# Kernel tuning notes

Measured on AMD Instinct MI355X. Metric: run time of the kernel, lower is better.

The kernel has to match this reference:

```python
import jax, jax.numpy as jnp
import numpy as np

NUM_HEADS = 16


def setup_inputs() -> dict:
    key = jax.random.key(0)
    ks = jax.random.split(key, 7)
    B, S, H = 2, 2048, 1024
    x = jax.random.normal(ks[0], (B, S, H), dtype=jnp.float32)
    y = jax.random.normal(ks[1], (B, S, H), dtype=jnp.float32)
    bias = jnp.zeros((B, 1, 1, S), dtype=jnp.float32)  # additive attention bias (padding mask)
    w_scale = 0.02
    wq = jax.random.normal(ks[2], (H, H), dtype=jnp.float32) * w_scale
    wk = jax.random.normal(ks[3], (H, H), dtype=jnp.float32) * w_scale
    wv = jax.random.normal(ks[4], (H, H), dtype=jnp.float32) * w_scale
    wo = jax.random.normal(ks[5], (H, H), dtype=jnp.float32) * w_scale
    return {"x": x, "y": y, "bias": bias, "wq": wq, "wk": wk, "wv": wv, "wo": wo}


def reference(x, y, bias, wq, wk, wv, wo):
    B, S, H = x.shape
    nh = NUM_HEADS
    dh = H // nh
    # QKV projections, split heads: [B, S, H] -> [B, nh, S, dh]
    q = jnp.einsum("bsh,hd->bsd", x, wq).reshape(B, S, nh, dh).transpose(0, 2, 1, 3)
    k = jnp.einsum("bsh,hd->bsd", y, wk).reshape(B, S, nh, dh).transpose(0, 2, 1, 3)
    v = jnp.einsum("bsh,hd->bsd", y, wv).reshape(B, S, nh, dh).transpose(0, 2, 1, 3)
    # Scale queries (tensor2tensor convention: q *= size_per_head ** -0.5)
    q = q * (dh ** -0.5)
    logits = jnp.einsum("bhqd,bhkd->bhqk", q, k) + bias  # [B, nh, S, S]
    weights = jax.nn.softmax(logits, axis=-1)
    # (attention_dropout = 0.0 -> identity)
    ctx = jnp.einsum("bhqk,bhkd->bhqd", weights, v)  # [B, nh, S, dh]
    ctx = ctx.transpose(0, 2, 1, 3).reshape(B, S, H)  # combine heads
    return jnp.einsum("bsh,hd->bsd", ctx, wo)
```

## Files before the change

kernel.cpp:

```cpp
#include <hip/hip_runtime.h>

using u16 = unsigned short;
using u32 = unsigned int;

typedef __bf16 bf16x8 __attribute__((ext_vector_type(8)));
typedef __bf16 bf16x4 __attribute__((ext_vector_type(4)));
typedef float f32x4 __attribute__((ext_vector_type(4)));
typedef u16 u16x4 __attribute__((ext_vector_type(4)));

#define GLD_LDS16(gp, lp)                                                                 \
  __builtin_amdgcn_global_load_lds((const __attribute__((address_space(1))) void*)(gp),   \
                                   (__attribute__((address_space(3))) void*)(lp), 16, 0, 0)

__device__ __forceinline__ u16 f2b(float f) {
  union { float f; u32 u; } v; v.f = f;
  return (u16)((v.u + 0x7fffu + ((v.u >> 16) & 1u)) >> 16);
}

__device__ __forceinline__ void pl32swap(u32& a, u32& b) {
  asm("v_permlane32_swap_b32 %0, %1" : "+v"(a), "+v"(b));
}
__device__ __forceinline__ void pl16swap(u32& a, u32& b) {
  asm("v_permlane16_swap_b32 %0, %1" : "+v"(a), "+v"(b));
}
__device__ __forceinline__ u32 cvtpk(float lo, float hi) {
  u32 d; asm("v_cvt_pk_bf16_f32 %0, %1, %2" : "=v"(d) : "v"(lo), "v"(hi));
  return d;
}

__global__ __launch_bounds__(256) void transpose4(
    const float* __restrict__ w0, const float* __restrict__ w1,
    const float* __restrict__ w2, const float* __restrict__ w3,
    u16* __restrict__ o0, u16* __restrict__ o1,
    u16* __restrict__ o2, u16* __restrict__ o3) {
  const float* src; u16* dst;
  switch (blockIdx.z) {
    case 0: src = w0; dst = o0; break;
    case 1: src = w1; dst = o1; break;
    case 2: src = w2; dst = o2; break;
    default: src = w3; dst = o3; break;
  }
  __shared__ float tile[64][65];
  int bx = blockIdx.x * 64, by = blockIdx.y * 64;
  int tx = threadIdx.x & 63, ty = threadIdx.x >> 6;
  for (int r = ty; r < 64; r += 4)
    tile[r][tx] = src[(size_t)(by + r) * 1024 + bx + tx];
  __syncthreads();
  for (int r = ty; r < 64; r += 4)
    dst[(size_t)(bx + r) * 1024 + by + tx] = f2b(tile[tx][r]);
}

__global__ __launch_bounds__(256) void cvt2bf16(
    const float* __restrict__ a, const float* __restrict__ b,
    u16* __restrict__ oa, u16* __restrict__ ob) {
  const float* src = blockIdx.y ? b : a;
  u16* dst = blockIdx.y ? ob : oa;
  size_t i = ((size_t)blockIdx.x * 256 + threadIdx.x) * 8;
  float4 f0 = *(const float4*)(src + i);
  float4 f1 = *(const float4*)(src + i + 4);
  bf16x8 v;
  v[0] = (__bf16)f0.x; v[1] = (__bf16)f0.y; v[2] = (__bf16)f0.z; v[3] = (__bf16)f0.w;
  v[4] = (__bf16)f1.x; v[5] = (__bf16)f1.y; v[6] = (__bf16)f1.z; v[7] = (__bf16)f1.w;
  *(bf16x8*)(dst + i) = v;
}

#define BM 128
#define BN 128
#define BK 64

__global__ __launch_bounds__(256) void gemm_qkv(
    const u16* __restrict__ xb, const u16* __restrict__ yb, const u16* __restrict__ wT,
    u16* __restrict__ Qb, u16* __restrict__ Kb, u16* __restrict__ Vb) {
  __shared__ __align__(16) u16 As[BM * BK];
  __shared__ __align__(16) u16 Bs[BN * BK];
  const int K = 1024;
  int region = blockIdx.y >> 3;
  const u16* A = (region == 0) ? xb : yb;
  const u16* BT = wT + (size_t)region * 1024 * 1024;
  float scale = (region == 0) ? 0.125f : 1.0f;
  int tid = threadIdx.x;
  int wave = tid >> 6, lane = tid & 63;
  int r = lane & 15, kg = lane >> 4;
  int bm = blockIdx.x * BM, bn = (blockIdx.y & 7) * BN;
  int wr = (wave >> 1) * 64, wc = (wave & 1) * 64;
  f32x4 acc[4][4] = {};

  const u16* Ag = A + (size_t)(bm + wave * 32 + (lane >> 3)) * K + (lane & 7) * 8;
  const u16* Bg = BT + (size_t)(bn + wave * 32 + (lane >> 3)) * K + (lane & 7) * 8;
  u16* Asb = As + wave * 32 * BK;
  u16* Bsb = Bs + wave * 32 * BK;

  for (int k0 = 0; k0 < K; k0 += BK) {
#pragma unroll
    for (int c = 0; c < 4; ++c) {
      GLD_LDS16(Ag + (size_t)c * 8 * K + k0, Asb + c * 8 * BK);
      GLD_LDS16(Bg + (size_t)c * 8 * K + k0, Bsb + c * 8 * BK);
    }
    __syncthreads();
#pragma unroll
    for (int kk = 0; kk < 2; ++kk) {
      bf16x8 af[4], bfv[4];
#pragma unroll
      for (int m = 0; m < 4; ++m)
        af[m] = *(const bf16x8*)&As[(wr + m * 16 + r) * BK + kk * 32 + kg * 8];
#pragma unroll
      for (int n = 0; n < 4; ++n)
        bfv[n] = *(const bf16x8*)&Bs[(wc + n * 16 + r) * BK + kk * 32 + kg * 8];
#pragma unroll
      for (int m = 0; m < 4; ++m)
#pragma unroll
        for (int n = 0; n < 4; ++n)
          acc[m][n] = __builtin_amdgcn_mfma_f32_16x16x32_bf16(af[m], bfv[n], acc[m][n], 0, 0, 0);
    }
    __syncthreads();
  }

  if (region == 2) {
#pragma unroll
    for (int m = 0; m < 4; ++m)
#pragma unroll
      for (int n = 0; n < 4; ++n) {
        int row0 = bm + wr + m * 16 + kg * 4;
        int col = bn + wc + n * 16 + r;
        int bb = row0 >> 11, s = row0 & 2047;
        int hh = col >> 6, dd = col & 63;
        u16x4 pk;
#pragma unroll
        for (int i = 0; i < 4; ++i) pk[i] = f2b(acc[m][n][i]);
        *(u16x4*)&Vb[((size_t)(bb * 16 + hh) * 64 + dd) * 2048 + s] = pk;
      }
  } else {
    u16* dst = (region == 0) ? Qb : Kb;
#pragma unroll
    for (int m = 0; m < 4; ++m)
#pragma unroll
      for (int n = 0; n < 4; ++n)
#pragma unroll
        for (int i = 0; i < 4; ++i) {
          int row = bm + wr + m * 16 + kg * 4 + i;
          int col = bn + wc + n * 16 + r;
          dst[(size_t)row * 1024 + col] = f2b(acc[m][n][i] * scale);
        }
  }
}

__global__ __launch_bounds__(256) void gemm_wo(
    const u16* __restrict__ A, const u16* __restrict__ BT, float* __restrict__ Cp,
    float scale) {
  __shared__ __align__(16) u16 As[BM * BK];
  __shared__ __align__(16) u16 Bs[64 * BK];
  const int K = 1024, N = 1024;
  int tid = threadIdx.x;
  int wave = tid >> 6, lane = tid & 63;
  int r = lane & 15, kg = lane >> 4;
  int lhi = lane >> 3, llo = lane & 7;
  int bm = blockIdx.x * BM, bn = blockIdx.y * 64;
  int wr = (wave >> 1) * 64, wc = (wave & 1) * 32;
  f32x4 acc[4][2] = {};

  const u16* Ag = A + (size_t)(bm + wave * 32 + lhi) * K + llo * 8;
  const u16* Bg = BT + (size_t)(bn + wave * 16 + lhi) * K + llo * 8;
  u16* Asb = As + wave * 32 * BK;
  u16* Bsb = Bs + wave * 16 * BK;

  for (int k0 = 0; k0 < K; k0 += BK) {
#pragma unroll
    for (int c = 0; c < 4; ++c)
      GLD_LDS16(Ag + (size_t)c * 8 * K + k0, Asb + c * 8 * BK);
#pragma unroll
    for (int c = 0; c < 2; ++c)
      GLD_LDS16(Bg + (size_t)c * 8 * K + k0, Bsb + c * 8 * BK);
    __syncthreads();
#pragma unroll
    for (int kk = 0; kk < 2; ++kk) {
      bf16x8 af[4], bfv[2];
#pragma unroll
      for (int m = 0; m < 4; ++m)
        af[m] = *(const bf16x8*)&As[(wr + m * 16 + r) * BK + kk * 32 + kg * 8];
#pragma unroll
      for (int n = 0; n < 2; ++n)
        bfv[n] = *(const bf16x8*)&Bs[(wc + n * 16 + r) * BK + kk * 32 + kg * 8];
#pragma unroll
      for (int m = 0; m < 4; ++m)
#pragma unroll
        for (int n = 0; n < 2; ++n)
          acc[m][n] = __builtin_amdgcn_mfma_f32_16x16x32_bf16(af[m], bfv[n], acc[m][n], 0, 0, 0);
    }
    __syncthreads();
  }

#pragma unroll
  for (int m = 0; m < 4; ++m)
#pragma unroll
    for (int n = 0; n < 2; ++n)
#pragma unroll
      for (int i = 0; i < 4; ++i) {
        int row = bm + wr + m * 16 + kg * 4 + i;
        int col = bn + wc + n * 16 + r;
        Cp[(size_t)row * N + col] = acc[m][n][i] * scale;
      }
}

__global__ __launch_bounds__(256) void flash_attn(
    const u16* __restrict__ Q, const u16* __restrict__ Km, const u16* __restrict__ VtG,
    const float* __restrict__ bias, u16* __restrict__ ctx) {
  const int S = 2048, H = 1024;
  __shared__ __align__(16) u16 Ks[2][64 * 64];
  __shared__ __align__(16) u16 Vs[2][64 * 64];
  int tid = threadIdx.x;
  int wave = tid >> 6, lane = tid & 63;
  int r = lane & 15, kg = lane >> 4;
  int h = blockIdx.x, b = blockIdx.y, qt = blockIdx.z;

  bf16x8 qa[2][2];
#pragma unroll
  for (int g = 0; g < 2; ++g) {
    const u16* Qb =
        Q + (size_t)(b * S + qt * 128 + g * 64 + wave * 16 + r) * H + h * 64 + kg * 8;
    qa[g][0] = *(const bf16x8*)(Qb);
    qa[g][1] = *(const bf16x8*)(Qb + 32);
  }

  int lhi = lane >> 3, llo = lane & 7;
  int ksch = llo ^ lhi;
  const u16* KgB = Km + (size_t)b * S * H + h * 64;
  const u16* VgB = VtG + ((size_t)(b * 16 + h) * 64) * 2048;
  const float* biasB = bias + (size_t)b * S;

  float m_i[2] = {-1e30f, -1e30f}, l_i[2] = {0.f, 0.f};
  f32x4 acc[2][4] = {};

  auto issueKV = [&](int kv0, int bi) {
#pragma unroll
    for (int c = 0; c < 2; ++c) {
      GLD_LDS16(KgB + (size_t)(kv0 + wave * 16 + c * 8 + lhi) * H + ksch * 8,
                &Ks[bi][wave * 16 * 64 + c * 8 * 64]);
      GLD_LDS16(VgB + (size_t)(wave * 16 + c * 8 + lhi) * 2048 + kv0 + ksch * 8,
                &Vs[bi][wave * 16 * 64 + c * 8 * 64]);
    }
  };
  auto issueB = [&](int kv0, f32x4* bv) {
#pragma unroll
    for (int n = 0; n < 4; ++n)
      bv[n] = *(const f32x4*)(biasB + kv0 + n * 16 + (kg << 2));
  };

  auto compute = [&](const u16* KsB, const u16* VsB, const f32x4* bv) {
#pragma unroll
    for (int g = 0; g < 2; ++g) {
      f32x4 sv[4] = {};
      __builtin_amdgcn_s_setprio(1);
#pragma unroll
      for (int kk = 0; kk < 2; ++kk)
#pragma unroll
        for (int n = 0; n < 4; ++n) {
          bf16x8 kb = *(const bf16x8*)&KsB[(n * 16 + r) * 64 +
                                           ((((kk << 2) + kg) ^ (r & 7)) << 3)];
          sv[n] = __builtin_amdgcn_mfma_f32_16x16x32_bf16(kb, qa[g][kk], sv[n], 0, 0, 0);
        }
      __builtin_amdgcn_s_setprio(0);

      f32x4 s4[4];
#pragma unroll
      for (int n = 0; n < 4; ++n) s4[n] = sv[n] + bv[n];
      float m0 = fmaxf(fmaxf(s4[0][0], s4[0][1]), fmaxf(s4[0][2], s4[0][3]));
      float m1 = fmaxf(fmaxf(s4[1][0], s4[1][1]), fmaxf(s4[1][2], s4[1][3]));
      float m2 = fmaxf(fmaxf(s4[2][0], s4[2][1]), fmaxf(s4[2][2], s4[2][3]));
      float m3 = fmaxf(fmaxf(s4[3][0], s4[3][1]), fmaxf(s4[3][2], s4[3][3]));
      float mx = fmaxf(fmaxf(m0, m1), fmaxf(m2, m3));
      mx = fmaxf(mx, __shfl_xor(mx, 16));
      mx = fmaxf(mx, __shfl_xor(mx, 32));
      float sc = 1.f;
      if (mx > m_i[g] + 8.f) { sc = __expf(m_i[g] - mx); l_i[g] *= sc; m_i[g] = mx; }
      if (__any(sc != 1.f)) {
#pragma unroll
        for (int i = 0; i < 4; ++i) {
          float sci = __shfl(sc, (lane & 48) | ((kg << 2) + i));
#pragma unroll
          for (int n = 0; n < 4; ++n) acc[g][n][i] *= sci;
        }
      }
      float rs = 0.f;
      float e[4][4];
#pragma unroll
      for (int n = 0; n < 4; ++n)
#pragma unroll
        for (int i = 0; i < 4; ++i) {
          e[n][i] = __expf(s4[n][i] - m_i[g]);
          rs += e[n][i];
        }
      rs += __shfl_xor(rs, 16);
      rs += __shfl_xor(rs, 32);
      l_i[g] += rs;

      u32 w[4][2];
#pragma unroll
      for (int n = 0; n < 4; ++n) {
        w[n][0] = cvtpk(e[n][0], e[n][1]);
        w[n][1] = cvtpk(e[n][2], e[n][3]);
      }

      __builtin_amdgcn_s_setprio(1);
#pragma unroll
      for (int kk = 0; kk < 2; ++kk) {
        u32 a0 = w[2 * kk][0], a1 = w[2 * kk][1];
        u32 b0 = w[2 * kk + 1][0], b1 = w[2 * kk + 1][1];
        pl32swap(a0, b0); pl32swap(a1, b1);
        pl16swap(a0, b0); pl16swap(a1, b1);
        union { u32 u[4]; bf16x8 v; } pa;
        pa.u[0] = a0; pa.u[1] = a1; pa.u[2] = b0; pa.u[3] = b1;
#pragma unroll
        for (int n = 0; n < 4; ++n) {
          bf16x8 vb = *(const bf16x8*)&VsB[(n * 16 + r) * 64 +
                                           ((((kk << 2) + kg) ^ (r & 7)) << 3)];
          acc[g][n] = __builtin_amdgcn_mfma_f32_16x16x32_bf16(pa.v, vb, acc[g][n], 0, 0, 0);
        }
      }
      __builtin_amdgcn_s_setprio(0);
    }
  };

  f32x4 bp[4], bn2[4];

  issueKV(0, 0); issueB(0, bp);
  __syncthreads();

  for (int t2 = 0; t2 < 16; ++t2) {
    int kv1 = (t2 * 2 + 1) * 64;
    int kv2 = ((t2 * 2 + 2) & 31) * 64;
    issueKV(kv1, 1); issueB(kv1, bn2);
    compute(Ks[0], Vs[0], bp);
    __syncthreads();
    issueKV(kv2, 0); issueB(kv2, bp);
    compute(Ks[1], Vs[1], bn2);
    __syncthreads();
  }

#pragma unroll
  for (int g = 0; g < 2; ++g)
#pragma unroll
    for (int i = 0; i < 4; ++i) {
      float li = __shfl(l_i[g], (lane & 48) | ((kg << 2) + i));
      float inv = 1.0f / li;
      size_t row = (size_t)(b * S + qt * 128 + g * 64 + wave * 16 + (kg << 2) + i);
#pragma unroll
      for (int n = 0; n < 4; ++n)
        ctx[row * H + h * 64 + n * 16 + r] = f2b(acc[g][n][i] * inv);
    }
}

extern "C" void kernel_launch(void* const* d_in, const int* in_sizes, int n_in,
                              void* d_out, int out_size, void* d_ws, size_t ws_size,
                              hipStream_t stream) {
  const float* x    = (const float*)d_in[0];
  const float* y    = (const float*)d_in[1];
  const float* bias = (const float*)d_in[2];
  const float* wq   = (const float*)d_in[3];
  const float* wk   = (const float*)d_in[4];
  const float* wv   = (const float*)d_in[5];
  const float* wo   = (const float*)d_in[6];
  float* out = (float*)d_out;

  u16* ws = (u16*)d_ws;
  const size_t WELEM = 1024 * 1024;
  const size_t MELEM = (size_t)4096 * 1024;
  u16* wqT = ws;
  u16* wkT = wqT + WELEM;
  u16* wvT = wkT + WELEM;
  u16* woT = wvT + WELEM;
  u16* Qb  = woT + WELEM;
  u16* Kb  = Qb + MELEM;
  u16* Vb  = Kb + MELEM;
  u16* xb  = Vb + MELEM;
  u16* yb  = xb + MELEM;
  u16* Cb  = Qb;

  dim3 blk(256);
  transpose4<<<dim3(16, 16, 4), blk, 0, stream>>>(wq, wk, wv, wo, wqT, wkT, wvT, woT);
  cvt2bf16<<<dim3(2048, 2), blk, 0, stream>>>(x, y, xb, yb);
  gemm_qkv<<<dim3(32, 24), blk, 0, stream>>>(xb, yb, wqT, Qb, Kb, Vb);
  flash_attn<<<dim3(16, 2, 16), blk, 0, stream>>>(Qb, Kb, Vb, bias, Cb);
  gemm_wo<<<dim3(32, 16), blk, 0, stream>>>(Cb, woT, out, 1.0f);
}
```

Before: 159.5 us.

## Merge weight transpose and activation cast into one launch; halve attention query tile

Folds the four weight transposes and the x/y bf16 casts into a single prep kernel, with the cast blocks looping grid-stride over the activations, which removes one kernel launch. The flash attention kernel now handles 64 query rows per block instead of 128 (one group per wave instead of two), doubling the grid to 1024 blocks for better CU occupancy and fewer registers per thread. The trade-off is that K/V tiles are loaded from global memory twice as often, since each block now reuses them across fewer queries.

```diff
diff --git a/kernel.cpp b/kernel.cpp
--- a/kernel.cpp
+++ b/kernel.cpp
@@ -28,40 +28,44 @@
   return d;
 }
 
-__global__ __launch_bounds__(256) void transpose4(
+__global__ __launch_bounds__(256) void prep(
     const float* __restrict__ w0, const float* __restrict__ w1,
     const float* __restrict__ w2, const float* __restrict__ w3,
     u16* __restrict__ o0, u16* __restrict__ o1,
-    u16* __restrict__ o2, u16* __restrict__ o3) {
-  const float* src; u16* dst;
-  switch (blockIdx.z) {
-    case 0: src = w0; dst = o0; break;
-    case 1: src = w1; dst = o1; break;
-    case 2: src = w2; dst = o2; break;
-    default: src = w3; dst = o3; break;
-  }
+    u16* __restrict__ o2, u16* __restrict__ o3,
+    const float* __restrict__ x, const float* __restrict__ y,
+    u16* __restrict__ xb, u16* __restrict__ yb) {
   __shared__ float tile[64][65];
-  int bx = blockIdx.x * 64, by = blockIdx.y * 64;
-  int tx = threadIdx.x & 63, ty = threadIdx.x >> 6;
-  for (int r = ty; r < 64; r += 4)
-    tile[r][tx] = src[(size_t)(by + r) * 1024 + bx + tx];
-  __syncthreads();
-  for (int r = ty; r < 64; r += 4)
-    dst[(size_t)(bx + r) * 1024 + by + tx] = f2b(tile[tx][r]);
-}
-
-__global__ __launch_bounds__(256) void cvt2bf16(
-    const float* __restrict__ a, const float* __restrict__ b,
-    u16* __restrict__ oa, u16* __restrict__ ob) {
-  const float* src = blockIdx.y ? b : a;
-  u16* dst = blockIdx.y ? ob : oa;
-  size_t i = ((size_t)blockIdx.x * 256 + threadIdx.x) * 8;
-  float4 f0 = *(const float4*)(src + i);
-  float4 f1 = *(const float4*)(src + i + 4);
-  bf16x8 v;
-  v[0] = (__bf16)f0.x; v[1] = (__bf16)f0.y; v[2] = (__bf16)f0.z; v[3] = (__bf16)f0.w;
-  v[4] = (__bf16)f1.x; v[5] = (__bf16)f1.y; v[6] = (__bf16)f1.z; v[7] = (__bf16)f1.w;
-  *(bf16x8*)(dst + i) = v;
+  int z = blockIdx.z;
+  if (z < 4) {
+    const float* src; u16* dst;
+    switch (z) {
+      case 0: src = w0; dst = o0; break;
+      case 1: src = w1; dst = o1; break;
+      case 2: src = w2; dst = o2; break;
+      default: src = w3; dst = o3; break;
+    }
+    int bx = blockIdx.x * 64, by = blockIdx.y * 64;
+    int tx = threadIdx.x & 63, ty = threadIdx.x >> 6;
+    for (int r = ty; r < 64; r += 4)
+      tile[r][tx] = src[(size_t)(by + r) * 1024 + bx + tx];
+    __syncthreads();
+    for (int r = ty; r < 64; r += 4)
+      dst[(size_t)(bx + r) * 1024 + by + tx] = f2b(tile[tx][r]);
+  } else {
+    const float* src = (z == 4) ? x : y;
+    u16* dst = (z == 4) ? xb : yb;
+    size_t base = ((size_t)(blockIdx.y * 16 + blockIdx.x) * 256 + threadIdx.x) * 8;
+    const size_t step = (size_t)256 * 256 * 8, total = (size_t)4096 * 1024;
+    for (size_t i = base; i < total; i += step) {
+      float4 f0 = *(const float4*)(src + i);
+      float4 f1 = *(const float4*)(src + i + 4);
+      bf16x8 v;
+      v[0] = (__bf16)f0.x; v[1] = (__bf16)f0.y; v[2] = (__bf16)f0.z; v[3] = (__bf16)f0.w;
+      v[4] = (__bf16)f1.x; v[5] = (__bf16)f1.y; v[6] = (__bf16)f1.z; v[7] = (__bf16)f1.w;
+      *(bf16x8*)(dst + i) = v;
+    }
+  }
 }
 
 #define BM 128
@@ -212,14 +216,10 @@
   int r = lane & 15, kg = lane >> 4;
   int h = blockIdx.x, b = blockIdx.y, qt = blockIdx.z;
 
-  bf16x8 qa[2][2];
-#pragma unroll
-  for (int g = 0; g < 2; ++g) {
-    const u16* Qb =
-        Q + (size_t)(b * S + qt * 128 + g * 64 + wave * 16 + r) * H + h * 64 + kg * 8;
-    qa[g][0] = *(const bf16x8*)(Qb);
-    qa[g][1] = *(const bf16x8*)(Qb + 32);
-  }
+  const u16* Qb = Q + (size_t)(b * S + qt * 64 + wave * 16 + r) * H + h * 64 + kg * 8;
+  bf16x8 qa[2];
+  qa[0] = *(const bf16x8*)(Qb);
+  qa[1] = *(const bf16x8*)(Qb + 32);
 
   int lhi = lane >> 3, llo = lane & 7;
   int ksch = llo ^ lhi;
@@ -227,8 +227,8 @@
   const u16* VgB = VtG + ((size_t)(b * 16 + h) * 64) * 2048;
   const float* biasB = bias + (size_t)b * S;
 
-  float m_i[2] = {-1e30f, -1e30f}, l_i[2] = {0.f, 0.f};
-  f32x4 acc[2][4] = {};
+  float m_i = -1e30f, l_i = 0.f;
+  f32x4 acc[4] = {};
 
   auto issueKV = [&](int kv0, int bi) {
 #pragma unroll
@@ -246,78 +246,75 @@
   };
 
   auto compute = [&](const u16* KsB, const u16* VsB, const f32x4* bv) {
-#pragma unroll
-    for (int g = 0; g < 2; ++g) {
-      f32x4 sv[4] = {};
-      __builtin_amdgcn_s_setprio(1);
-#pragma unroll
-      for (int kk = 0; kk < 2; ++kk)
-#pragma unroll
-        for (int n = 0; n < 4; ++n) {
-          bf16x8 kb = *(const bf16x8*)&KsB[(n * 16 + r) * 64 +
-                                           ((((kk << 2) + kg) ^ (r & 7)) << 3)];
-          sv[n] = __builtin_amdgcn_mfma_f32_16x16x32_bf16(kb, qa[g][kk], sv[n], 0, 0, 0);
-        }
-      __builtin_amdgcn_s_setprio(0);
-
-      f32x4 s4[4];
-#pragma unroll
-      for (int n = 0; n < 4; ++n) s4[n] = sv[n] + bv[n];
-      float m0 = fmaxf(fmaxf(s4[0][0], s4[0][1]), fmaxf(s4[0][2], s4[0][3]));
-      float m1 = fmaxf(fmaxf(s4[1][0], s4[1][1]), fmaxf(s4[1][2], s4[1][3]));
-      float m2 = fmaxf(fmaxf(s4[2][0], s4[2][1]), fmaxf(s4[2][2], s4[2][3]));
-      float m3 = fmaxf(fmaxf(s4[3][0], s4[3][1]), fmaxf(s4[3][2], s4[3][3]));
-      float mx = fmaxf(fmaxf(m0, m1), fmaxf(m2, m3));
-      mx = fmaxf(mx, __shfl_xor(mx, 16));
-      mx = fmaxf(mx, __shfl_xor(mx, 32));
-      float sc = 1.f;
-      if (mx > m_i[g] + 8.f) { sc = __expf(m_i[g] - mx); l_i[g] *= sc; m_i[g] = mx; }
-      if (__any(sc != 1.f)) {
-#pragma unroll
-        for (int i = 0; i < 4; ++i) {
-          float sci = __shfl(sc, (lane & 48) | ((kg << 2) + i));
-#pragma unroll
-          for (int n = 0; n < 4; ++n) acc[g][n][i] *= sci;
-        }
-      }
-      float rs = 0.f;
-      float e[4][4];
-#pragma unroll
-      for (int n = 0; n < 4; ++n)
-#pragma unroll
-        for (int i = 0; i < 4; ++i) {
-          e[n][i] = __expf(s4[n][i] - m_i[g]);
-          rs += e[n][i];
-        }
-      rs += __shfl_xor(rs, 16);
-      rs += __shfl_xor(rs, 32);
-      l_i[g] += rs;
-
-      u32 w[4][2];
+    f32x4 sv[4] = {};
+    __builtin_amdgcn_s_setprio(1);
+#pragma unroll
+    for (int kk = 0; kk < 2; ++kk)
 #pragma unroll
       for (int n = 0; n < 4; ++n) {
-        w[n][0] = cvtpk(e[n][0], e[n][1]);
-        w[n][1] = cvtpk(e[n][2], e[n][3]);
-      }
-
-      __builtin_amdgcn_s_setprio(1);
-#pragma unroll
-      for (int kk = 0; kk < 2; ++kk) {
-        u32 a0 = w[2 * kk][0], a1 = w[2 * kk][1];
-        u32 b0 = w[2 * kk + 1][0], b1 = w[2 * kk + 1][1];
-        pl32swap(a0, b0); pl32swap(a1, b1);
-        pl16swap(a0, b0); pl16swap(a1, b1);
-        union { u32 u[4]; bf16x8 v; } pa;
-        pa.u[0] = a0; pa.u[1] = a1; pa.u[2] = b0; pa.u[3] = b1;
-#pragma unroll
-        for (int n = 0; n < 4; ++n) {
-          bf16x8 vb = *(const bf16x8*)&VsB[(n * 16 + r) * 64 +
-                                           ((((kk << 2) + kg) ^ (r & 7)) << 3)];
-          acc[g][n] = __builtin_amdgcn_mfma_f32_16x16x32_bf16(pa.v, vb, acc[g][n], 0, 0, 0);
-        }
-      }
-      __builtin_amdgcn_s_setprio(0);
-    }
+        bf16x8 kb = *(const bf16x8*)&KsB[(n * 16 + r) * 64 +
+                                         ((((kk << 2) + kg) ^ (r & 7)) << 3)];
+        sv[n] = __builtin_amdgcn_mfma_f32_16x16x32_bf16(kb, qa[kk], sv[n], 0, 0, 0);
+      }
+    __builtin_amdgcn_s_setprio(0);
+
+    f32x4 s4[4];
+#pragma unroll
+    for (int n = 0; n < 4; ++n) s4[n] = sv[n] + bv[n];
+    float m0 = fmaxf(fmaxf(s4[0][0], s4[0][1]), fmaxf(s4[0][2], s4[0][3]));
+    float m1 = fmaxf(fmaxf(s4[1][0], s4[1][1]), fmaxf(s4[1][2], s4[1][3]));
+    float m2 = fmaxf(fmaxf(s4[2][0], s4[2][1]), fmaxf(s4[2][2], s4[2][3]));
+    float m3 = fmaxf(fmaxf(s4[3][0], s4[3][1]), fmaxf(s4[3][2], s4[3][3]));
+    float mx = fmaxf(fmaxf(m0, m1), fmaxf(m2, m3));
+    mx = fmaxf(mx, __shfl_xor(mx, 16));
+    mx = fmaxf(mx, __shfl_xor(mx, 32));
+    float sc = 1.f;
+    if (mx > m_i + 8.f) { sc = __expf(m_i - mx); l_i *= sc; m_i = mx; }
+    if (__any(sc != 1.f)) {
+#pragma unroll
+      for (int i = 0; i < 4; ++i) {
+        float sci = __shfl(sc, (lane & 48) | ((kg << 2) + i));
+#pragma unroll
+        for (int n = 0; n < 4; ++n) acc[n][i] *= sci;
+      }
+    }
+    float rs = 0.f;
+    float e[4][4];
+#pragma unroll
+    for (int n = 0; n < 4; ++n)
+#pragma unroll
+      for (int i = 0; i < 4; ++i) {
+        e[n][i] = __expf(s4[n][i] - m_i);
+        rs += e[n][i];
+      }
+    rs += __shfl_xor(rs, 16);
+    rs += __shfl_xor(rs, 32);
+    l_i += rs;
+
+    u32 w[4][2];
+#pragma unroll
+    for (int n = 0; n < 4; ++n) {
+      w[n][0] = cvtpk(e[n][0], e[n][1]);
+      w[n][1] = cvtpk(e[n][2], e[n][3]);
+    }
+
+    __builtin_amdgcn_s_setprio(1);
+#pragma unroll
+    for (int kk = 0; kk < 2; ++kk) {
+      u32 a0 = w[2 * kk][0], a1 = w[2 * kk][1];
+      u32 b0 = w[2 * kk + 1][0], b1 = w[2 * kk + 1][1];
+      pl32swap(a0, b0); pl32swap(a1, b1);
+      pl16swap(a0, b0); pl16swap(a1, b1);
+      union { u32 u[4]; bf16x8 v; } pa;
+      pa.u[0] = a0; pa.u[1] = a1; pa.u[2] = b0; pa.u[3] = b1;
+#pragma unroll
+      for (int n = 0; n < 4; ++n) {
+        bf16x8 vb = *(const bf16x8*)&VsB[(n * 16 + r) * 64 +
+                                         ((((kk << 2) + kg) ^ (r & 7)) << 3)];
+        acc[n] = __builtin_amdgcn_mfma_f32_16x16x32_bf16(pa.v, vb, acc[n], 0, 0, 0);
+      }
+    }
+    __builtin_amdgcn_s_setprio(0);
   };
 
   f32x4 bp[4], bn2[4];
@@ -337,16 +334,14 @@
   }
 
 #pragma unroll
-  for (int g = 0; g < 2; ++g)
-#pragma unroll
-    for (int i = 0; i < 4; ++i) {
-      float li = __shfl(l_i[g], (lane & 48) | ((kg << 2) + i));
-      float inv = 1.0f / li;
-      size_t row = (size_t)(b * S + qt * 128 + g * 64 + wave * 16 + (kg << 2) + i);
-#pragma unroll
-      for (int n = 0; n < 4; ++n)
-        ctx[row * H + h * 64 + n * 16 + r] = f2b(acc[g][n][i] * inv);
-    }
+  for (int i = 0; i < 4; ++i) {
+    float li = __shfl(l_i, (lane & 48) | ((kg << 2) + i));
+    float inv = 1.0f / li;
+    size_t row = (size_t)(b * S + qt * 64 + wave * 16 + (kg << 2) + i);
+#pragma unroll
+    for (int n = 0; n < 4; ++n)
+      ctx[row * H + h * 64 + n * 16 + r] = f2b(acc[n][i] * inv);
+  }
 }
 
 extern "C" void kernel_launch(void* const* d_in, const int* in_sizes, int n_in,
@@ -376,9 +371,9 @@
   u16* Cb  = Qb;
 
   dim3 blk(256);
-  transpose4<<<dim3(16, 16, 4), blk, 0, stream>>>(wq, wk, wv, wo, wqT, wkT, wvT, woT);
-  cvt2bf16<<<dim3(2048, 2), blk, 0, stream>>>(x, y, xb, yb);
+  prep<<<dim3(16, 16, 6), blk, 0, stream>>>(wq, wk, wv, wo, wqT, wkT, wvT, woT,
+                                            x, y, xb, yb);
   gemm_qkv<<<dim3(32, 24), blk, 0, stream>>>(xb, yb, wqT, Qb, Kb, Vb);
-  flash_attn<<<dim3(16, 2, 16), blk, 0, stream>>>(Qb, Kb, Vb, bias, Cb);
+  flash_attn<<<dim3(16, 2, 32), blk, 0, stream>>>(Qb, Kb, Vb, bias, Cb);
   gemm_wo<<<dim3(32, 16), blk, 0, stream>>>(Cb, woT, out, 1.0f);
 }
```

Result: no change. 158.9 us (-0.3%).

## Merge prep kernels, fold log2e into Q scale, use permlane reductions

Applied to the files above, without the earlier changes.

Merges the weight transpose and the x/y bf16 conversion into one prep launch, which also pre-scales the bias by log2(e). The Q projection scale also absorbs log2(e), so flash attention can call exp2f directly instead of __expf. The cross-lane max and sum reductions switch from shuffles to permlane32/16 swaps. This removes one launch and some per-element multiplies and shuffle latency. It adds a small bias buffer, and the conversion now uses a grid-stride loop over fewer blocks.

```diff
diff --git a/kernel.cpp b/kernel.cpp
--- a/kernel.cpp
+++ b/kernel.cpp
@@ -27,41 +27,72 @@
   u32 d; asm("v_cvt_pk_bf16_f32 %0, %1, %2" : "=v"(d) : "v"(lo), "v"(hi));
   return d;
 }
-
-__global__ __launch_bounds__(256) void transpose4(
+__device__ __forceinline__ float red4_max(float x) {
+  union { float f; u32 u; } a, b;
+  a.f = x;
+  asm("v_mov_b32 %0, %1" : "=v"(b.u) : "v"(a.u));
+  asm("v_permlane32_swap_b32 %0, %1" : "+v"(a.u), "+v"(b.u));
+  union { float f; u32 u; } m, c;
+  m.f = fmaxf(a.f, b.f);
+  asm("v_mov_b32 %0, %1" : "=v"(c.u) : "v"(m.u));
+  asm("v_permlane16_swap_b32 %0, %1" : "+v"(m.u), "+v"(c.u));
+  return fmaxf(m.f, c.f);
+}
+__device__ __forceinline__ float red4_sum(float x) {
+  union { float f; u32 u; } a, b;
+  a.f = x;
+  asm("v_mov_b32 %0, %1" : "=v"(b.u) : "v"(a.u));
+  asm("v_permlane32_swap_b32 %0, %1" : "+v"(a.u), "+v"(b.u));
+  union { float f; u32 u; } m, c;
+  m.f = a.f + b.f;
+  asm("v_mov_b32 %0, %1" : "=v"(c.u) : "v"(m.u));
+  asm("v_permlane16_swap_b32 %0, %1" : "+v"(m.u), "+v"(c.u));
+  return m.f + c.f;
+}
+
+__global__ __launch_bounds__(256) void prep(
     const float* __restrict__ w0, const float* __restrict__ w1,
     const float* __restrict__ w2, const float* __restrict__ w3,
     u16* __restrict__ o0, u16* __restrict__ o1,
-    u16* __restrict__ o2, u16* __restrict__ o3) {
-  const float* src; u16* dst;
-  switch (blockIdx.z) {
-    case 0: src = w0; dst = o0; break;
-    case 1: src = w1; dst = o1; break;
-    case 2: src = w2; dst = o2; break;
-    default: src = w3; dst = o3; break;
-  }
+    u16* __restrict__ o2, u16* __restrict__ o3,
+    const float* __restrict__ x, const float* __restrict__ y,
+    u16* __restrict__ xb, u16* __restrict__ yb,
+    const float* __restrict__ bias, float* __restrict__ bs) {
   __shared__ float tile[64][65];
-  int bx = blockIdx.x * 64, by = blockIdx.y * 64;
-  int tx = threadIdx.x & 63, ty = threadIdx.x >> 6;
-  for (int r = ty; r < 64; r += 4)
-    tile[r][tx] = src[(size_t)(by + r) * 1024 + bx + tx];
-  __syncthreads();
-  for (int r = ty; r < 64; r += 4)
-    dst[(size_t)(bx + r) * 1024 + by + tx] = f2b(tile[tx][r]);
-}
-
-__global__ __launch_bounds__(256) void cvt2bf16(
-    const float* __restrict__ a, const float* __restrict__ b,
-    u16* __restrict__ oa, u16* __restrict__ ob) {
-  const float* src = blockIdx.y ? b : a;
-  u16* dst = blockIdx.y ? ob : oa;
-  size_t i = ((size_t)blockIdx.x * 256 + threadIdx.x) * 8;
-  float4 f0 = *(const float4*)(src + i);
-  float4 f1 = *(const float4*)(src + i + 4);
-  bf16x8 v;
-  v[0] = (__bf16)f0.x; v[1] = (__bf16)f0.y; v[2] = (__bf16)f0.z; v[3] = (__bf16)f0.w;
-  v[4] = (__bf16)f1.x; v[5] = (__bf16)f1.y; v[6] = (__bf16)f1.z; v[7] = (__bf16)f1.w;
-  *(bf16x8*)(dst + i) = v;
+  int z = blockIdx.z;
+  if (z < 4) {
+    const float* src; u16* dst;
+    switch (z) {
+      case 0: src = w0; dst = o0; break;
+      case 1: src = w1; dst = o1; break;
+      case 2: src = w2; dst = o2; break;
+      default: src = w3; dst = o3; break;
+    }
+    int bx = blockIdx.x * 64, by = blockIdx.y * 64;
+    int tx = threadIdx.x & 63, ty = threadIdx.x >> 6;
+    for (int r = ty; r < 64; r += 4)
+      tile[r][tx] = src[(size_t)(by + r) * 1024 + bx + tx];
+    __syncthreads();
+    for (int r = ty; r < 64; r += 4)
+      dst[(size_t)(bx + r) * 1024 + by + tx] = f2b(tile[tx][r]);
+  } else if (z < 6) {
+    const float* src = (z == 4) ? x : y;
+    u16* dst = (z == 4) ? xb : yb;
+    size_t base = ((size_t)(blockIdx.y * 16 + blockIdx.x) * 256 + threadIdx.x) * 8;
+    const size_t step = (size_t)256 * 256 * 8, total = (size_t)4096 * 1024;
+    for (size_t i = base; i < total; i += step) {
+      float4 f0 = *(const float4*)(src + i);
+      float4 f1 = *(const float4*)(src + i + 4);
+      bf16x8 v;
+      v[0] = (__bf16)f0.x; v[1] = (__bf16)f0.y; v[2] = (__bf16)f0.z; v[3] = (__bf16)f0.w;
+      v[4] = (__bf16)f1.x; v[5] = (__bf16)f1.y; v[6] = (__bf16)f1.z; v[7] = (__bf16)f1.w;
+      *(bf16x8*)(dst + i) = v;
+    }
+  } else {
+    if (blockIdx.x == 0 && blockIdx.y == 0)
+      for (int i = threadIdx.x; i < 4096; i += 256)
+        bs[i] = bias[i] * 1.44269504088896f;
+  }
 }
 
 #define BM 128
@@ -77,7 +108,7 @@
   int region = blockIdx.y >> 3;
   const u16* A = (region == 0) ? xb : yb;
   const u16* BT = wT + (size_t)region * 1024 * 1024;
-  float scale = (region == 0) ? 0.125f : 1.0f;
+  float scale = (region == 0) ? 0.125f * 1.44269504088896f : 1.0f;
   int tid = threadIdx.x;
   int wave = tid >> 6, lane = tid & 63;
   int r = lane & 15, kg = lane >> 4;
@@ -203,7 +234,7 @@
 
 __global__ __launch_bounds__(256) void flash_attn(
     const u16* __restrict__ Q, const u16* __restrict__ Km, const u16* __restrict__ VtG,
-    const float* __restrict__ bias, u16* __restrict__ ctx) {
+    const float* __restrict__ biasS, u16* __restrict__ ctx) {
   const int S = 2048, H = 1024;
   __shared__ __align__(16) u16 Ks[2][64 * 64];
   __shared__ __align__(16) u16 Vs[2][64 * 64];
@@ -225,7 +256,7 @@
   int ksch = llo ^ lhi;
   const u16* KgB = Km + (size_t)b * S * H + h * 64;
   const u16* VgB = VtG + ((size_t)(b * 16 + h) * 64) * 2048;
-  const float* biasB = bias + (size_t)b * S;
+  const float* biasB = biasS + (size_t)b * S;
 
   float m_i[2] = {-1e30f, -1e30f}, l_i[2] = {0.f, 0.f};
   f32x4 acc[2][4] = {};
@@ -267,11 +298,9 @@
       float m1 = fmaxf(fmaxf(s4[1][0], s4[1][1]), fmaxf(s4[1][2], s4[1][3]));
       float m2 = fmaxf(fmaxf(s4[2][0], s4[2][1]), fmaxf(s4[2][2], s4[2][3]));
       float m3 = fmaxf(fmaxf(s4[3][0], s4[3][1]), fmaxf(s4[3][2], s4[3][3]));
-      float mx = fmaxf(fmaxf(m0, m1), fmaxf(m2, m3));
-      mx = fmaxf(mx, __shfl_xor(mx, 16));
-      mx = fmaxf(mx, __shfl_xor(mx, 32));
+      float mx = red4_max(fmaxf(fmaxf(m0, m1), fmaxf(m2, m3)));
       float sc = 1.f;
-      if (mx > m_i[g] + 8.f) { sc = __expf(m_i[g] - mx); l_i[g] *= sc; m_i[g] = mx; }
+      if (mx > m_i[g] + 8.f) { sc = exp2f(m_i[g] - mx); l_i[g] *= sc; m_i[g] = mx; }
       if (__any(sc != 1.f)) {
 #pragma unroll
         for (int i = 0; i < 4; ++i) {
@@ -286,12 +315,10 @@
       for (int n = 0; n < 4; ++n)
 #pragma unroll
         for (int i = 0; i < 4; ++i) {
-          e[n][i] = __expf(s4[n][i] - m_i[g]);
+          e[n][i] = exp2f(s4[n][i] - m_i[g]);
           rs += e[n][i];
         }
-      rs += __shfl_xor(rs, 16);
-      rs += __shfl_xor(rs, 32);
-      l_i[g] += rs;
+      l_i[g] += red4_sum(rs);
 
       u32 w[4][2];
 #pragma unroll
@@ -373,12 +400,13 @@
   u16* Vb  = Kb + MELEM;
   u16* xb  = Vb + MELEM;
   u16* yb  = xb + MELEM;
+  float* bs = (float*)(yb + MELEM);
   u16* Cb  = Qb;
 
   dim3 blk(256);
-  transpose4<<<dim3(16, 16, 4), blk, 0, stream>>>(wq, wk, wv, wo, wqT, wkT, wvT, woT);
-  cvt2bf16<<<dim3(2048, 2), blk, 0, stream>>>(x, y, xb, yb);
+  prep<<<dim3(16, 16, 7), blk, 0, stream>>>(wq, wk, wv, wo, wqT, wkT, wvT, woT,
+                                            x, y, xb, yb, bias, bs);
   gemm_qkv<<<dim3(32, 24), blk, 0, stream>>>(xb, yb, wqT, Qb, Kb, Vb);
-  flash_attn<<<dim3(16, 2, 16), blk, 0, stream>>>(Qb, Kb, Vb, bias, Cb);
+  flash_attn<<<dim3(16, 2, 16), blk, 0, stream>>>(Qb, Kb, Vb, bs, Cb);
   gemm_wo<<<dim3(32, 16), blk, 0, stream>>>(Cb, woT, out, 1.0f);
 }
```

New measurement: 169.2 us. 6.1% more time.
